# Optimization experiments

Measured on AMD Instinct MI355X. Metric: run time of the kernel, lower is better.

Reference implementation:

```python
import jax, jax.numpy as jnp
import numpy as np

B, Z, H, T = 256, 512, 1024, 512   # batch, z_size, hidden (conductor==decoder), num_tokens
L, N = 16, 16                      # num_levels, notes_per_bar


def setup_inputs() -> dict:
    key = jax.random.key(0)
    ks = jax.random.split(key, 16)
    s = 0.05  # weight init scale
    rn = lambda k, shp, sc=1.0: sc * jax.random.normal(k, shp, dtype=jnp.float32)
    return {
        "z": rn(ks[0], (B, L * N, 1, Z)),
        "dec_h0": rn(ks[1], (L, B, H)),
        "dec_c0": rn(ks[2], (L, B, H)),
        # linear_in (computed but unused by the original forward)
        "lin_in_W": rn(ks[3], (Z, Z), s), "lin_in_b": rn(ks[4], (Z,), s),
        # conductor LSTM (input Z -> hidden H), PyTorch gate order i,f,g,o
        "cond_Wih": rn(ks[5], (4 * H, Z), s), "cond_Whh": rn(ks[6], (4 * H, H), s),
        "cond_bih": rn(ks[7], (4 * H,), s), "cond_bhh": rn(ks[8], (4 * H,), s),
        # decoder LSTM (input T+H -> hidden H)
        "dec_Wih": rn(ks[9], (4 * H, T + H), s), "dec_Whh": rn(ks[10], (4 * H, H), s),
        "dec_bih": rn(ks[11], (4 * H,), s), "dec_bhh": rn(ks[12], (4 * H,), s),
        # output projection
        "out_W": rn(ks[13], (T, H), s), "out_b": rn(ks[14], (T,), s),
    }


def _lstm_cell(x, h, c, Wih, Whh, b):
    gates = x @ Wih.T + h @ Whh.T + b            # [B, 4H]
    i, f, g, o = jnp.split(gates, 4, axis=-1)
    c = jax.nn.sigmoid(f) * c + jax.nn.sigmoid(i) * jnp.tanh(g)
    h = jax.nn.sigmoid(o) * jnp.tanh(c)
    return h, c


def reference(z, dec_h0, dec_c0, lin_in_W, lin_in_b,
              cond_Wih, cond_Whh, cond_bih, cond_bhh,
              dec_Wih, dec_Whh, dec_bih, dec_bhh, out_W, out_b):
    Bsz = z.shape[0]
    Tt = out_b.shape[0]
    Hh = cond_Whh.shape[1]

    _unused = z @ lin_in_W.T + lin_in_b  # linear_in output is discarded in the source

    cond_b = cond_bih + cond_bhh
    dec_b = dec_bih + dec_bhh

    # conductor consumes z[:, L*level, 0, :] for each level
    z_lv = jnp.transpose(z[:, jnp.arange(L) * L, 0, :], (1, 0, 2))  # [L, B, Z]

    def level_step(carry, xs):
        ch, cc = carry
        zl, dh, dc = xs
        ch, cc = _lstm_cell(zl, ch, cc, cond_Wih, cond_Whh, cond_b)
        emb = ch  # [B, H], fixed conductor embedding for this bar

        def note_step(c2, _):
            note, dh2, dc2 = c2
            inp = jnp.concatenate([emb, note], axis=-1)  # [B, H+T]
            dh2, dc2 = _lstm_cell(inp, dh2, dc2, dec_Wih, dec_Whh, dec_b)
            out = jax.nn.sigmoid(dh2 @ out_W.T + out_b)  # [B, T]
            return (out, dh2, dc2), out

        note0 = jnp.zeros((Bsz, Tt), dtype=z.dtype)
        _, outs = jax.lax.scan(note_step, (note0, dh, dc), None, length=N)  # [N, B, T]
        return (ch, cc), outs

    h0 = jnp.zeros((Bsz, Hh), dtype=z.dtype)
    _, all_outs = jax.lax.scan(level_step, (h0, h0), (z_lv, dec_h0, dec_c0))  # [L, N, B, T]
    notes = jnp.transpose(all_outs, (2, 0, 1, 3)).reshape(Bsz, L * N, Tt)
    return notes
```

## Files before the change

kernel.cpp:

```cpp
#include <hip/hip_runtime.h>

typedef __bf16 bf16;
typedef __attribute__((ext_vector_type(8))) __bf16 bf16x8;
typedef __attribute__((ext_vector_type(4))) float f32x4;
typedef __attribute__((ext_vector_type(4))) unsigned short u16x4;

__device__ __forceinline__ void gload_lds16(const void* g, void* l) {
  __builtin_amdgcn_global_load_lds(
      (const __attribute__((address_space(1))) void*)g,
      (__attribute__((address_space(3))) void*)l, 16, 0, 0);
}

__device__ __forceinline__ float sigmoidf_(float x) { return 1.0f / (1.0f + expf(-x)); }

__device__ __forceinline__ float bf2f(unsigned short u) {
  union { unsigned int i; float f; } v;
  v.i = ((unsigned int)u) << 16;
  return v.f;
}
__device__ __forceinline__ unsigned short f2bfbits(float x) {
  union { bf16 b; unsigned short u; } v;
  v.b = (bf16)x;
  return v.u;
}

#define SB() __builtin_amdgcn_sched_barrier(0)
#define MFMA16(a, b, c) __builtin_amdgcn_mfma_f32_16x16x32_bf16(a, b, c, 0, 0, 0)

template<int MODE>
__global__ __launch_bounds__(512, 2)
void gemm8(const bf16* __restrict__ A, int lda,
           const bf16* __restrict__ Bw, int K,
           bf16* __restrict__ Cb,
           const bf16* __restrict__ X, const float* __restrict__ bias,
           float* __restrict__ cst, bf16* __restrict__ hout, int ldh) {
  extern __shared__ __align__(16) char smem_raw[];
  bf16* lsA = (bf16*)smem_raw;
  bf16* lsB = lsA + 4 * 8192;

  const int tid = threadIdx.x;
  const int lane = tid & 63;
  const int wave = tid >> 6;
  const int wm = wave >> 2, wn = wave & 3;

  const int bid = blockIdx.x;
  const int wgid = (bid & 7) * 32 + (bid >> 3);
  const int m0 = (wgid >> 4) * 256, n0 = (wgid & 15) * 256;

  const int nkt = K >> 5;

  const int srow = tid >> 2;
  const int scol = ((tid & 3) ^ ((srow >> 1) & 3)) * 8;
  const bf16* gAs = A + (size_t)(m0 + srow) * lda + scol;
  const bf16* gBs = Bw + (size_t)(n0 + srow) * K + scol;

  auto stA = [&](int kt) {
    bf16* d = lsA + (kt & 3) * 8192 + tid * 8;
    const bf16* s = gAs + (size_t)kt * 32;
    gload_lds16(s, d);
    gload_lds16(s + (size_t)128 * lda, d + 4096);
  };
  auto stB = [&](int kt) {
    bf16* d = lsB + (kt & 3) * 8192 + tid * 8;
    const bf16* s = gBs + (size_t)kt * 32;
    gload_lds16(s, d);
    gload_lds16(s + (size_t)128 * K, d + 4096);
  };

  const int sw = ((lane & 15) >> 1) & 3;
  const int rslot = ((lane >> 4) ^ sw) * 8;
  const int abase = (wm * 128 + (lane & 15)) * 32 + rslot;
  const int bbase = (wn * 64 + (lane & 15)) * 32 + rslot;

  f32x4 acc[8][4] = {};

  stA(0); stB(0); stA(1); stB(1);
  asm volatile("s_waitcnt vmcnt(4)" ::: "memory");

  for (int t = 0; t < nkt; ++t) {
    SB();
    __builtin_amdgcn_s_barrier();
    SB();
    const bf16* pA = lsA + (t & 3) * 8192;
    const bf16* pB = lsB + (t & 3) * 8192;
    bf16x8 av[8], bv[4];
#pragma unroll
    for (int f = 0; f < 8; ++f) av[f] = *(const bf16x8*)&pA[abase + f * 512];
#pragma unroll
    for (int g = 0; g < 4; ++g) bv[g] = *(const bf16x8*)&pB[bbase + g * 512];
    if (t + 2 < nkt) { stA(t + 2); stB(t + 2); }
    asm volatile("s_waitcnt lgkmcnt(0)" ::: "memory");
    SB();
    __builtin_amdgcn_s_setprio(1);
#pragma unroll
    for (int f = 0; f < 8; ++f)
#pragma unroll
      for (int g = 0; g < 4; ++g)
        acc[f][g] = MFMA16(av[f], bv[g], acc[f][g]);
    __builtin_amdgcn_s_setprio(0);
    if (t + 2 < nkt)      asm volatile("s_waitcnt vmcnt(4)" ::: "memory");
    else if (t + 1 < nkt) asm volatile("s_waitcnt vmcnt(0)" ::: "memory");
  }

  const int jj = lane & 15;
  const int rb = m0 + wm * 128 + ((lane >> 4) << 2);
  const int q = (n0 >> 6) + wn;
  if constexpr (MODE == 0) {
#pragma unroll
    for (int f = 0; f < 8; ++f)
#pragma unroll
      for (int r = 0; r < 4; ++r) {
        u16x4 pk;
        pk[0] = f2bfbits(acc[f][0][r]);
        pk[1] = f2bfbits(acc[f][1][r]);
        pk[2] = f2bfbits(acc[f][2][r]);
        pk[3] = f2bfbits(acc[f][3][r]);
        *(u16x4*)&Cb[(size_t)(rb + f * 16 + r) * 4096 + q * 64 + jj * 4] = pk;
      }
  } else {
    const int j = q * 16 + jj;
    const f32x4 bq = *(const f32x4*)&bias[q * 64 + jj * 4];
#pragma unroll
    for (int f = 0; f < 8; ++f) {
#pragma unroll
      for (int r = 0; r < 4; ++r) {
        const int row = rb + f * 16 + r;
        const u16x4 xv = *(const u16x4*)&X[(size_t)row * 4096 + q * 64 + jj * 4];
        const float gi = acc[f][0][r] + bf2f(xv[0]) + bq[0];
        const float gf = acc[f][1][r] + bf2f(xv[1]) + bq[1];
        const float gg = acc[f][2][r] + bf2f(xv[2]) + bq[2];
        const float go = acc[f][3][r] + bf2f(xv[3]) + bq[3];
        const size_t ci = (size_t)row * 1024 + j;
        const float cn = sigmoidf_(gf) * cst[ci] + sigmoidf_(gi) * tanhf(gg);
        cst[ci] = cn;
        hout[(size_t)row * ldh + j] = (bf16)(sigmoidf_(go) * tanhf(cn));
      }
    }
  }
}

template<int BM, int BN, int WM, int WN, int MODE>
__global__ __launch_bounds__(WM * WN * 64)
void gemm_bt(const bf16* __restrict__ A, int lda,
             const bf16* __restrict__ Bw, int ldb,
             float* __restrict__ C, int ldc, int K,
             const float* __restrict__ outb, float* __restrict__ dout,
             bf16* __restrict__ anote, int nstep) {
  constexpr int BK = 64;
  constexpr int THREADS = WM * WN * 64;
  constexpr int SM = BM / WM, SN = BN / WN;
  constexpr int FM = SM / 16, FN = SN / 16;

  __shared__ __align__(16) bf16 lsA[BM * BK];
  __shared__ __align__(16) bf16 lsB[BN * BK];

  const int tid = threadIdx.x;
  const int lane = tid & 63;
  const int wave = tid >> 6;
  const int wm = wave / WN, wn = wave % WN;
  const int m0 = blockIdx.y * BM;
  const int n0 = blockIdx.x * BN;

  f32x4 acc[FM][FN] = {};

  const bf16* gA = A + (size_t)m0 * lda;
  const bf16* gB = Bw + (size_t)n0 * ldb;

  for (int k0 = 0; k0 < K; k0 += BK) {
#pragma unroll
    for (int i = 0; i < (BM * 8) / THREADS; ++i) {
      int idx = i * THREADS + tid;
      gload_lds16(gA + (size_t)(idx >> 3) * lda + k0 + (idx & 7) * 8, &lsA[idx * 8]);
    }
#pragma unroll
    for (int i = 0; i < (BN * 8) / THREADS; ++i) {
      int idx = i * THREADS + tid;
      gload_lds16(gB + (size_t)(idx >> 3) * ldb + k0 + (idx & 7) * 8, &lsB[idx * 8]);
    }
    __syncthreads();

#pragma unroll
    for (int kk = 0; kk < BK; kk += 32) {
      bf16x8 av[FM], bv[FN];
#pragma unroll
      for (int i = 0; i < FM; ++i)
        av[i] = *(const bf16x8*)&lsA[(wm * SM + i * 16 + (lane & 15)) * BK + kk + (lane >> 4) * 8];
#pragma unroll
      for (int j = 0; j < FN; ++j)
        bv[j] = *(const bf16x8*)&lsB[(wn * SN + j * 16 + (lane & 15)) * BK + kk + (lane >> 4) * 8];
#pragma unroll
      for (int i = 0; i < FM; ++i)
#pragma unroll
        for (int j = 0; j < FN; ++j)
          acc[i][j] = MFMA16(av[i], bv[j], acc[i][j]);
    }
    __syncthreads();
  }

#pragma unroll
  for (int i = 0; i < FM; ++i) {
#pragma unroll
    for (int j = 0; j < FN; ++j) {
      const int col = n0 + wn * SN + j * 16 + (lane & 15);
      const int rbase = m0 + wm * SM + i * 16 + ((lane >> 4) << 2);
#pragma unroll
      for (int r = 0; r < 4; ++r) {
        const int row = rbase + r;
        float v = acc[i][j][r];
        if constexpr (MODE == 0) {
          C[(size_t)row * ldc + col] = v;
        } else {
          v = sigmoidf_(v + outb[col]);
          const int l = row >> 8, b = row & 255;
          dout[((size_t)(b * 256 + l * 16 + nstep)) * 512 + col] = v;
          anote[(size_t)row * 1536 + col] = (bf16)v;
        }
      }
    }
  }
}

template<int BM, int BJ, int WM, int WJ>
__global__ __launch_bounds__(WM * WJ * 64, 2)
void gemm_cell(const bf16* __restrict__ A, int lda,
               const bf16* __restrict__ Bw,
               const bf16* __restrict__ X,
               const float* __restrict__ bias,
               float* __restrict__ cst,
               bf16* __restrict__ hout, int ldh, int K) {
  constexpr int BK = 64;
  constexpr int THREADS = WM * WJ * 64;
  constexpr int BN = BJ * 64;
  constexpr int SM = BM / WM;
  constexpr int TJ = BJ / WJ;
  constexpr int FM = SM / 16;

  __shared__ __align__(16) bf16 lsA[BM * BK];
  __shared__ __align__(16) bf16 lsB[BN * BK];

  const int tid = threadIdx.x;
  const int lane = tid & 63;
  const int wave = tid >> 6;
  const int wm = wave / WJ, wj = wave % WJ;
  const int m0 = blockIdx.y * BM;
  const int qb = blockIdx.x * BJ;

  f32x4 acc[FM][TJ][4] = {};

  const bf16* gA = A + (size_t)m0 * lda;
  const bf16* gB = Bw + (size_t)(qb * 64) * K;

  for (int k0 = 0; k0 < K; k0 += BK) {
#pragma unroll
    for (int i = 0; i < (BM * 8) / THREADS; ++i) {
      int idx = i * THREADS + tid;
      gload_lds16(gA + (size_t)(idx >> 3) * lda + k0 + (idx & 7) * 8, &lsA[idx * 8]);
    }
#pragma unroll
    for (int i = 0; i < (BN * 8) / THREADS; ++i) {
      int idx = i * THREADS + tid;
      gload_lds16(gB + (size_t)(idx >> 3) * K + k0 + (idx & 7) * 8, &lsB[idx * 8]);
    }
    __syncthreads();

#pragma unroll
    for (int kk = 0; kk < BK; kk += 32) {
      bf16x8 av[FM], bv[TJ][4];
#pragma unroll
      for (int i = 0; i < FM; ++i)
        av[i] = *(const bf16x8*)&lsA[(wm * SM + i * 16 + (lane & 15)) * BK + kk + (lane >> 4) * 8];
#pragma unroll
      for (int t = 0; t < TJ; ++t)
#pragma unroll
        for (int g = 0; g < 4; ++g)
          bv[t][g] = *(const bf16x8*)
              &lsB[((wj * TJ + t) * 64 + g * 16 + (lane & 15)) * BK + kk + (lane >> 4) * 8];
#pragma unroll
      for (int i = 0; i < FM; ++i)
#pragma unroll
        for (int t = 0; t < TJ; ++t)
#pragma unroll
          for (int g = 0; g < 4; ++g)
            acc[i][t][g] = MFMA16(av[i], bv[t][g], acc[i][t][g]);
    }
    __syncthreads();
  }

#pragma unroll
  for (int i = 0; i < FM; ++i) {
#pragma unroll
    for (int t = 0; t < TJ; ++t) {
      const int q = qb + wj * TJ + t;
      const int jj = lane & 15;
      const int j = q * 16 + jj;
      const int rbase = m0 + wm * SM + i * 16 + ((lane >> 4) << 2);
      const f32x4 bq = *(const f32x4*)&bias[q * 64 + jj * 4];
#pragma unroll
      for (int r = 0; r < 4; ++r) {
        const int row = rbase + r;
        const u16x4 xv = *(const u16x4*)&X[(size_t)row * 4096 + q * 64 + jj * 4];
        const float gi = acc[i][t][0][r] + bf2f(xv[0]) + bq[0];
        const float gf = acc[i][t][1][r] + bf2f(xv[1]) + bq[1];
        const float gg = acc[i][t][2][r] + bf2f(xv[2]) + bq[2];
        const float go = acc[i][t][3][r] + bf2f(xv[3]) + bq[3];
        const size_t ci = (size_t)row * 1024 + j;
        const float c = sigmoidf_(gf) * cst[ci] + sigmoidf_(gi) * tanhf(gg);
        cst[ci] = c;
        hout[(size_t)row * ldh + j] = (bf16)(sigmoidf_(go) * tanhf(c));
      }
    }
  }
}


__device__ __forceinline__ u16x4 f4_to_bf4(f32x4 v) {
  u16x4 o;
  o[0] = f2bfbits(v[0]); o[1] = f2bfbits(v[1]);
  o[2] = f2bfbits(v[2]); o[3] = f2bfbits(v[3]);
  return o;
}

__device__ __forceinline__ int p_src_row(int n) {
  int q = n >> 6, gate = (n >> 4) & 3, jj = n & 15;
  return gate * 1024 + q * 16 + jj;
}

__global__ void conv_f32_bf16_4(const float* __restrict__ src, bf16* __restrict__ dst) {
  int idx = (blockIdx.x * 256 + threadIdx.x) * 4;
  *(u16x4*)&dst[idx] = f4_to_bf4(*(const f32x4*)&src[idx]);
}

__global__ void pack_w_dec(const float* __restrict__ wih, const float* __restrict__ whh,
                           bf16* __restrict__ dst) {
  int idx = (blockIdx.x * 256 + threadIdx.x) * 4;
  int n = idx / 1536, c = idx - n * 1536;
  int r = p_src_row(n);
  const float* s = (c < 512) ? &wih[(size_t)r * 1536 + 1024 + c]
                             : &whh[(size_t)r * 1024 + (c - 512)];
  *(u16x4*)&dst[idx] = f4_to_bf4(*(const f32x4*)s);
}

__global__ void pack_w_emb(const float* __restrict__ wih, bf16* __restrict__ dst) {
  int idx = (blockIdx.x * 256 + threadIdx.x) * 4;
  int n = idx >> 10, c = idx & 1023;
  *(u16x4*)&dst[idx] = f4_to_bf4(*(const f32x4*)&wih[(size_t)p_src_row(n) * 1536 + c]);
}

__global__ void pack_w_perm(const float* __restrict__ src, bf16* __restrict__ dst, int Kw) {
  int idx = (blockIdx.x * 256 + threadIdx.x) * 4;
  int n = idx / Kw, c = idx - n * Kw;
  *(u16x4*)&dst[idx] = f4_to_bf4(*(const f32x4*)&src[(size_t)p_src_row(n) * Kw + c]);
}

__global__ void pack_bias(const float* __restrict__ bih, const float* __restrict__ bhh,
                          float* __restrict__ dst) {
  int n = blockIdx.x * 256 + threadIdx.x;
  int q = n >> 6, jj = (n >> 2) & 15, g = n & 3;
  int r = g * 1024 + q * 16 + jj;
  dst[n] = bih[r] + bhh[r];
}

__global__ void pack_zb(const float* __restrict__ z, bf16* __restrict__ dst) {
  int idx = (blockIdx.x * 256 + threadIdx.x) * 4;
  int m = idx >> 9, k = idx & 511;
  int l = m >> 8, b = m & 255;
  *(u16x4*)&dst[idx] =
      f4_to_bf4(*(const f32x4*)&z[((size_t)b * 256 + 16 * l) * 512 + k]);
}

__global__ void init_cond(float* __restrict__ cc, bf16* __restrict__ hz0) {
  int idx = (blockIdx.x * 256 + threadIdx.x) * 4;
  *(f32x4*)&cc[idx] = f32x4{0.f, 0.f, 0.f, 0.f};
  *(u16x4*)&hz0[idx] = u16x4{0, 0, 0, 0};
}

__global__ void init_state(const float* __restrict__ h0, const float* __restrict__ c0,
                           bf16* __restrict__ Abuf, float* __restrict__ cdec) {
  int idx = (blockIdx.x * 256 + threadIdx.x) * 4;
  int m = idx / 1536, c = idx - m * 1536;
  if (c < 512) {
    *(u16x4*)&Abuf[idx] = u16x4{0, 0, 0, 0};
  } else {
    int j = c - 512;
    size_t s = (size_t)m * 1024 + j;
    f32x4 h = *(const f32x4*)&h0[s];
    *(u16x4*)&Abuf[idx] = f4_to_bf4(h);
    *(f32x4*)&cdec[s] = *(const f32x4*)&c0[s];
  }
}

extern "C" void kernel_launch(void* const* d_in, const int* in_sizes, int n_in,
                              void* d_out, int out_size, void* d_ws, size_t ws_size,
                              hipStream_t stream) {
  const float* z        = (const float*)d_in[0];
  const float* dec_h0   = (const float*)d_in[1];
  const float* dec_c0   = (const float*)d_in[2];
  const float* cond_Wih = (const float*)d_in[5];
  const float* cond_Whh = (const float*)d_in[6];
  const float* cond_bih = (const float*)d_in[7];
  const float* cond_bhh = (const float*)d_in[8];
  const float* dec_Wih  = (const float*)d_in[9];
  const float* dec_Whh  = (const float*)d_in[10];
  const float* dec_bih  = (const float*)d_in[11];
  const float* dec_bhh  = (const float*)d_in[12];
  const float* out_W    = (const float*)d_in[13];
  const float* out_b    = (const float*)d_in[14];
  float* out = (float*)d_out;

  char* ws = (char*)d_ws;
  size_t off = 0;
  auto alloc = [&](size_t bytes) {
    void* p = ws + off;
    off += (bytes + 255) & ~(size_t)255;
    return p;
  };
  bf16* E     = (bf16*)alloc(4096ull * 4096 * 2);
  bf16* Xz    = (bf16*)alloc(4096ull * 4096 * 2);
  float* cdec = (float*)alloc(4096ull * 1024 * 4);
  bf16* Ab0   = (bf16*)alloc(4096ull * 1536 * 2);
  bf16* Ab1   = (bf16*)alloc(4096ull * 1536 * 2);
  bf16* Wd    = (bf16*)alloc(4096ull * 1536 * 2);
  bf16* We    = (bf16*)alloc(4096ull * 1024 * 2);
  bf16* Wcih  = (bf16*)alloc(4096ull * 512 * 2);
  bf16* Wchh  = (bf16*)alloc(4096ull * 1024 * 2);
  bf16* Wo    = (bf16*)alloc(512ull * 1024 * 2);
  float* cc   = (float*)alloc(256ull * 1024 * 4);
  bf16* emb   = (bf16*)alloc(4096ull * 1024 * 2);
  bf16* Zb    = (bf16*)alloc(4096ull * 512 * 2);
  bf16* hz0   = (bf16*)alloc(256ull * 1024 * 2);
  float* bdP  = (float*)alloc(4096ull * 4);
  float* bcP  = (float*)alloc(4096ull * 4);

  dim3 b256(256);

  hipFuncSetAttribute(reinterpret_cast<const void*>(&gemm8<0>),
                      hipFuncAttributeMaxDynamicSharedMemorySize, 131072);
  hipFuncSetAttribute(reinterpret_cast<const void*>(&gemm8<1>),
                      hipFuncAttributeMaxDynamicSharedMemorySize, 131072);

  pack_w_perm<<<4096 * 512 / 1024, b256, 0, stream>>>(cond_Wih, Wcih, 512);
  pack_w_perm<<<4096 * 1024 / 1024, b256, 0, stream>>>(cond_Whh, Wchh, 1024);
  conv_f32_bf16_4<<<512 * 1024 / 1024, b256, 0, stream>>>(out_W, Wo);
  pack_w_dec<<<4096 * 1536 / 1024, b256, 0, stream>>>(dec_Wih, dec_Whh, Wd);
  pack_w_emb<<<4096 * 1024 / 1024, b256, 0, stream>>>(dec_Wih, We);
  pack_bias<<<16, b256, 0, stream>>>(dec_bih, dec_bhh, bdP);
  pack_bias<<<16, b256, 0, stream>>>(cond_bih, cond_bhh, bcP);
  pack_zb<<<4096 * 512 / 1024, b256, 0, stream>>>(z, Zb);
  init_cond<<<256 * 1024 / 1024, b256, 0, stream>>>(cc, hz0);
  init_state<<<4096 * 1536 / 1024, b256, 0, stream>>>(dec_h0, dec_c0, Ab0, cdec);

  gemm8<0><<<256, 512, 131072, stream>>>(Zb, 512, Wcih, 512, Xz,
                                         nullptr, nullptr, nullptr, nullptr, 0);

  for (int l = 0; l < 16; ++l) {
    const bf16* hprev = (l == 0) ? hz0 : (emb + (size_t)(l - 1) * 256 * 1024);
    gemm_cell<32, 2, 2, 2><<<dim3(32, 8), dim3(256), 0, stream>>>(
        hprev, 1024, Wchh, Xz + (size_t)l * 256 * 4096, bcP,
        cc, emb + (size_t)l * 256 * 1024, 1024, 1024);
  }

  gemm8<0><<<256, 512, 131072, stream>>>(emb, 1024, We, 1024, E,
                                         nullptr, nullptr, nullptr, nullptr, 0);

  for (int n = 0; n < 16; ++n) {
    bf16* Sc = (n & 1) ? Ab1 : Ab0;
    bf16* Sn = (n & 1) ? Ab0 : Ab1;
    gemm8<1><<<256, 512, 131072, stream>>>(Sc, 1536, Wd, 1536, nullptr,
                                           E, bdP, cdec, Sn + 512, 1536);
    gemm_bt<128, 64, 2, 2, 1><<<dim3(512 / 64, 4096 / 128), dim3(256), 0, stream>>>(
        Sn + 512, 1536, Wo, 1024, nullptr, 0, 1024, out_b, out, Sn, n);
  }
}
```

Before: 1.734 ms.

## Store decoder cell state in bf16 and remap block indices for L2 locality

Changes the decoder LSTM cell state buffer from fp32 to bf16, which halves the read/write traffic for the cell state in the fused gate epilogue on every step. It also remaps workgroup-to-tile assignment in gemm8 (swapping m/n tile roles) and adds swizzled block orderings in two gemm kernels so that blocks running together share operand tiles in cache. Keeping the cell state in bf16 loses precision, and the error can build up across the recurrent steps.

```diff
diff --git a/kernel.cpp b/kernel.cpp
--- a/kernel.cpp
+++ b/kernel.cpp
@@ -33,7 +33,7 @@
            const bf16* __restrict__ Bw, int K,
            bf16* __restrict__ Cb,
            const bf16* __restrict__ X, const float* __restrict__ bias,
-           float* __restrict__ cst, bf16* __restrict__ hout, int ldh) {
+           bf16* __restrict__ cst, bf16* __restrict__ hout, int ldh) {
   extern __shared__ __align__(16) char smem_raw[];
   bf16* lsA = (bf16*)smem_raw;
   bf16* lsB = lsA + 4 * 8192;
@@ -45,7 +45,7 @@
 
   const int bid = blockIdx.x;
   const int wgid = (bid & 7) * 32 + (bid >> 3);
-  const int m0 = (wgid >> 4) * 256, n0 = (wgid & 15) * 256;
+  const int m0 = (wgid & 15) * 256, n0 = (wgid >> 4) * 256;
 
   const int nkt = K >> 5;
 
@@ -131,8 +131,9 @@
         const float gg = acc[f][2][r] + bf2f(xv[2]) + bq[2];
         const float go = acc[f][3][r] + bf2f(xv[3]) + bq[3];
         const size_t ci = (size_t)row * 1024 + j;
-        const float cn = sigmoidf_(gf) * cst[ci] + sigmoidf_(gi) * tanhf(gg);
-        cst[ci] = cn;
+        const float cold = bf2f(((const unsigned short*)cst)[ci]);
+        const float cn = sigmoidf_(gf) * cold + sigmoidf_(gi) * tanhf(gg);
+        cst[ci] = (bf16)cn;
         hout[(size_t)row * ldh + j] = (bf16)(sigmoidf_(go) * tanhf(cn));
       }
     }
@@ -158,8 +159,15 @@
   const int lane = tid & 63;
   const int wave = tid >> 6;
   const int wm = wave / WN, wn = wave % WN;
-  const int m0 = blockIdx.y * BM;
-  const int n0 = blockIdx.x * BN;
+
+  int mi = blockIdx.y, ni = blockIdx.x;
+  if constexpr (MODE == 1) {
+    const int flat = blockIdx.y * 8 + blockIdx.x;
+    mi = (flat & 7) * 4 + ((flat >> 3) & 3);
+    ni = flat >> 5;
+  }
+  const int m0 = mi * BM;
+  const int n0 = ni * BN;
 
   f32x4 acc[FM][FN] = {};
 
@@ -242,8 +250,15 @@
   const int lane = tid & 63;
   const int wave = tid >> 6;
   const int wm = wave / WJ, wj = wave % WJ;
-  const int m0 = blockIdx.y * BM;
-  const int qb = blockIdx.x * BJ;
+
+  int qbi = blockIdx.x, mi = blockIdx.y;
+  if constexpr (BM == 32 && BJ == 2) {
+    const int flat = blockIdx.y * 32 + blockIdx.x;
+    qbi = (flat & 7) * 4 + ((flat >> 3) & 3);
+    mi = flat >> 5;
+  }
+  const int m0 = mi * BM;
+  const int qb = qbi * BJ;
 
   f32x4 acc[FM][TJ][4] = {};
 
@@ -375,7 +390,7 @@
 }
 
 __global__ void init_state(const float* __restrict__ h0, const float* __restrict__ c0,
-                           bf16* __restrict__ Abuf, float* __restrict__ cdec) {
+                           bf16* __restrict__ Abuf, bf16* __restrict__ cdec) {
   int idx = (blockIdx.x * 256 + threadIdx.x) * 4;
   int m = idx / 1536, c = idx - m * 1536;
   if (c < 512) {
@@ -383,9 +398,8 @@
   } else {
     int j = c - 512;
     size_t s = (size_t)m * 1024 + j;
-    f32x4 h = *(const f32x4*)&h0[s];
-    *(u16x4*)&Abuf[idx] = f4_to_bf4(h);
-    *(f32x4*)&cdec[s] = *(const f32x4*)&c0[s];
+    *(u16x4*)&Abuf[idx] = f4_to_bf4(*(const f32x4*)&h0[s]);
+    *(u16x4*)&cdec[s] = f4_to_bf4(*(const f32x4*)&c0[s]);
   }
 }
 
@@ -416,7 +430,7 @@
   };
   bf16* E     = (bf16*)alloc(4096ull * 4096 * 2);
   bf16* Xz    = (bf16*)alloc(4096ull * 4096 * 2);
-  float* cdec = (float*)alloc(4096ull * 1024 * 4);
+  bf16* cdec  = (bf16*)alloc(4096ull * 1024 * 2);
   bf16* Ab0   = (bf16*)alloc(4096ull * 1536 * 2);
   bf16* Ab1   = (bf16*)alloc(4096ull * 1536 * 2);
   bf16* Wd    = (bf16*)alloc(4096ull * 1536 * 2);
```

Measured after the change: 1.693 ms, median of 3. 1.02x faster.
